# Optimization experiments

Measured on AMD Instinct MI355X. Metric: run time of the kernel, lower is better.

Reference implementation:

```python
import jax, jax.numpy as jnp
import numpy as np

B, S, DIM = 4, 2048, 512
HEADS, DHEAD = 8, 64
INNER = HEADS * DHEAD


def setup_inputs() -> dict:
    key = jax.random.key(0)
    k1, k2, k3, k4 = jax.random.split(key, 4)
    x = jax.random.normal(k1, (B, S, DIM), dtype=jnp.float32)
    W_qkv = jax.random.normal(k2, (DIM, 3 * INNER), dtype=jnp.float32) * (DIM ** -0.5)
    W_out = jax.random.normal(k3, (INNER, DIM), dtype=jnp.float32) * (INNER ** -0.5)
    b_out = jnp.zeros((DIM,), dtype=jnp.float32)
    # learnable log-temperature, initialized to log(dim_head**-0.5)
    log_temp = jnp.asarray(np.log(DHEAD ** -0.5), dtype=jnp.float32)
    return {"x": x, "W_qkv": W_qkv, "log_temp": log_temp, "W_out": W_out, "b_out": b_out}


def reference(x, W_qkv, log_temp, W_out, b_out):
    b, s, _ = x.shape
    qkv = x @ W_qkv  # [b, s, 3*inner]
    q, k, v = jnp.split(qkv, 3, axis=-1)
    # [b, s, inner] -> [b, h, s, d]
    reshape = lambda t: t.reshape(b, s, HEADS, DHEAD).transpose(0, 2, 1, 3)
    q, k, v = reshape(q), reshape(k), reshape(v)
    dots = jnp.einsum("bhid,bhjd->bhij", q, k) * jnp.exp(log_temp)
    mask_value = -jnp.finfo(dots.dtype).max
    eye = jnp.eye(s, dtype=bool)
    dots = jnp.where(eye, mask_value, dots)
    attn = jax.nn.softmax(dots, axis=-1)
    out = jnp.einsum("bhij,bhjd->bhid", attn, v)
    out = out.transpose(0, 2, 1, 3).reshape(b, s, INNER)
    return out @ W_out + b_out
```

## Files before the change

### kernel.cpp

```cpp
#include <hip/hip_runtime.h>
#include <hip/hip_bf16.h>

#define BB 4
#define SS 2048
#define DIMM 512
#define HH 8
#define DD 64
#define NQKV 1536

typedef float  floatx4 __attribute__((ext_vector_type(4)));
typedef short  bf16x8  __attribute__((ext_vector_type(8)));
typedef short  bf16x4  __attribute__((ext_vector_type(4)));

#define MFMA16(A, B, C) __builtin_amdgcn_mfma_f32_16x16x32_bf16(A, B, C, 0, 0, 0)

__device__ __forceinline__ floatx4 MFMA16K16(bf16x4 a, bf16x4 b, floatx4 c) {
#if __has_builtin(__builtin_amdgcn_mfma_f32_16x16x16bf16_1k)
    return __builtin_amdgcn_mfma_f32_16x16x16bf16_1k(a, b, c, 0, 0, 0);
#else
    floatx4 d;
    asm volatile("v_mfma_f32_16x16x16_bf16 %0, %1, %2, %3"
                 : "=v"(d) : "v"(a), "v"(b), "v"(c));
    return d;
#endif
}

__device__ __forceinline__ unsigned short f2bf(float f) {
    unsigned int u = __float_as_uint(f);
    u += 0x7FFFu + ((u >> 16) & 1u);
    return (unsigned short)(u >> 16);
}

__device__ __forceinline__ unsigned int f2bf_pk(float lo, float hi) {
    float2 f; f.x = lo; f.y = hi;
    __hip_bfloat162 h = __float22bfloat162_rn(f);
    return *reinterpret_cast<unsigned int*>(&h);
}

__device__ __forceinline__ float fast_exp2(float x) {
#if __has_builtin(__builtin_amdgcn_exp2f)
    return __builtin_amdgcn_exp2f(x);
#else
    return __exp2f(x);
#endif
}

__device__ __forceinline__ void gl_lds16(const void* g, void* l) {
    __builtin_amdgcn_global_load_lds(
        (__attribute__((address_space(1))) void*)g,
        (__attribute__((address_space(3))) void*)l,
        16, 0, 0);
}

__global__ __launch_bounds__(256) void k_prep(
    const float* __restrict__ x, const float* __restrict__ W_qkv,
    const float* __restrict__ W_out,
    unsigned short* __restrict__ xb, unsigned short* __restrict__ Wq_t,
    unsigned short* __restrict__ Wo_t) {
    __shared__ float t[32][33];
    int bid = blockIdx.x, tid = threadIdx.x;
    if (bid < 4096) {
        int i = (bid * 256 + tid) * 4;
        float4 v = *(const float4*)(x + i);
        ushort4 o;
        o.x = f2bf(v.x); o.y = f2bf(v.y); o.z = f2bf(v.z); o.w = f2bf(v.w);
        *(ushort4*)(xb + i) = o;
        return;
    }
    const float* in; unsigned short* out; int R = 512, C, bx, by;
    if (bid < 4864) { in = W_qkv; out = Wq_t; C = 1536; int blk = bid - 4096; bx = blk % 48; by = blk / 48; }
    else            { in = W_out; out = Wo_t; C = 512;  int blk = bid - 4864; bx = blk % 16; by = blk / 16; }
    int tx = tid & 31, ty = tid >> 5;
    int c0 = bx * 32, r0 = by * 32;
    for (int i = 0; i < 4; i++) {
        int r = r0 + ty + i * 8;
        t[ty + i * 8][tx] = in[(size_t)r * C + c0 + tx];
    }
    __syncthreads();
    for (int i = 0; i < 4; i++) {
        int cc = c0 + ty + i * 8;
        out[(size_t)cc * R + r0 + tx] = f2bf(t[tx][ty + i * 8]);
    }
}

__global__ __launch_bounds__(256) void k_gemm_qkv(
    const unsigned short* __restrict__ A,
    const unsigned short* __restrict__ Bt,
    const float* __restrict__ log_temp,
    unsigned short* __restrict__ Qb,
    unsigned short* __restrict__ Kb,
    unsigned short* __restrict__ Vt) {
    __shared__ unsigned short smem[2][128 * 64];
    unsigned short* As = smem[0];
    unsigned short* Bs = smem[1];
    const int K = 512;
    int m0 = blockIdx.x * 128, n0 = blockIdx.y * 128;
    int tid = threadIdx.x;
    int w = tid >> 6, lane = tid & 63;
    int c = lane & 15, q4 = lane >> 4;
    int wm = w >> 1, wn = w & 1;
    float qscale = __expf(log_temp[0]) * 1.44269504f;

    floatx4 acc[4][4] = {};

    for (int k0 = 0; k0 < K; k0 += 64) {
        __syncthreads();
        for (int i = 0; i < 4; i++) {
            int cidx = w * 256 + i * 64 + lane;
            int row = cidx >> 3, cc = cidx & 7;
            int gcc = cc ^ (row & 7);
            gl_lds16(A + (size_t)(m0 + row) * K + k0 + gcc * 8,
                     As + (size_t)(w * 256 + i * 64) * 8);
            gl_lds16(Bt + (size_t)(n0 + row) * K + k0 + gcc * 8,
                     Bs + (size_t)(w * 256 + i * 64) * 8);
        }
        __syncthreads();
        bf16x8 aF[2][4], bF[2][4];
        for (int kh = 0; kh < 2; kh++)
            for (int mt = 0; mt < 4; mt++) {
                int row = wm * 64 + mt * 16 + c;
                aF[kh][mt] = *(const bf16x8*)&As[row * 64 + (((kh * 4 + q4) ^ (row & 7)) * 8)];
            }
        for (int kh = 0; kh < 2; kh++)
            for (int nt = 0; nt < 4; nt++) {
                int row = wn * 64 + nt * 16 + c;
                bF[kh][nt] = *(const bf16x8*)&Bs[row * 64 + (((kh * 4 + q4) ^ (row & 7)) * 8)];
            }
        for (int kh = 0; kh < 2; kh++)
            for (int mt = 0; mt < 4; mt++)
                for (int nt = 0; nt < 4; nt++)
                    acc[mt][nt] = MFMA16(aF[kh][mt], bF[kh][nt], acc[mt][nt]);
    }

    if (n0 < 1024) {
        for (int nt = 0; nt < 4; nt++) {
            int n = n0 + wn * 64 + nt * 16 + c;
            int t = n >> 9, inner = n & 511;
            int h = inner >> 6, d = inner & 63;
            for (int mt = 0; mt < 4; mt++) {
                for (int r = 0; r < 4; r++) {
                    int m = m0 + wm * 64 + mt * 16 + q4 * 4 + r;
                    int b = m >> 11, s = m & 2047;
                    int bh = b * 8 + h;
                    float v = acc[mt][nt][r];
                    if (t == 0)  Qb[((size_t)bh * SS + s) * 64 + d] = f2bf(v * qscale);
                    else         Kb[((size_t)bh * SS + s) * 64 + d] = f2bf(v);
                }
            }
        }
    } else {
        unsigned short* T = &smem[0][0];
        int b = m0 >> 11, s_base = m0 & 2047;
        for (int half = 0; half < 2; half++) {
            __syncthreads();
            if (wn == half) {
                for (int nt = 0; nt < 4; nt++)
                    for (int mt = 0; mt < 4; mt++)
                        for (int r = 0; r < 4; r++)
                            T[(nt * 16 + c) * 136 + wm * 64 + mt * 16 + q4 * 4 + r] =
                                f2bf(acc[mt][nt][r]);
            }
            __syncthreads();
            for (int rr = 0; rr < 4; rr++) {
                int nl = w * 16 + rr * 4 + q4;
                int ml = c * 8;
                bf16x8 v = *(const bf16x8*)&T[nl * 136 + ml];
                int n = n0 + half * 64 + nl;
                int h = (n >> 6) - 16, d = n & 63;
                int bh = b * 8 + h;
                *(bf16x8*)(Vt + ((size_t)bh * 64 + d) * SS + s_base + ml) = v;
            }
        }
    }
}

__global__ __launch_bounds__(512, 4) void k_attn(
    const unsigned short* __restrict__ Qb,
    const unsigned short* __restrict__ Kb,
    const unsigned short* __restrict__ Vt,
    unsigned short* __restrict__ AO) {
    __shared__ unsigned short Ks[2][64 * 64];
    __shared__ unsigned short Vs[2][64 * 64];
    int q0 = blockIdx.x * 128;
    int h = blockIdx.y, b = blockIdx.z;
    int bh = b * 8 + h;
    int tid = threadIdx.x, w = tid >> 6, lane = tid & 63;
    int c = lane & 15, q4 = lane >> 4;

    const unsigned short* Kbase = Kb + (size_t)bh * SS * 64;
    const unsigned short* Vbase = Vt + (size_t)bh * 64 * SS;

    bf16x8 qf[2];
    {
        const unsigned short* qp = Qb + ((size_t)bh * SS + q0 + w * 16 + c) * 64;
        qf[0] = *(const bf16x8*)(qp + q4 * 8);
        qf[1] = *(const bf16x8*)(qp + 32 + q4 * 8);
    }

    int grow = tid >> 3, gcc = (tid & 7) ^ (grow & 7);
    const unsigned short* ksrc = Kbase + (size_t)grow * 64 + gcc * 8;
    const unsigned short* vsrc = Vbase + (size_t)grow * SS + gcc * 8;
    unsigned short* kdst = (unsigned short*)Ks[0] + w * 512;
    unsigned short* vdst = (unsigned short*)Vs[0] + w * 512;

    gl_lds16(ksrc, kdst);
    gl_lds16(vsrc, vdst);

    int mask_j0 = (q0 + w * 16) & ~63;
    int mglob = q0 + w * 16 + c;
    floatx4 oacc[4] = {};
    float psum = 0.f;

    for (int j0 = 0; j0 < SS; j0 += 64) {
        int buf = (j0 >> 6) & 1;
        __syncthreads();
        if (j0 + 64 < SS) {
            gl_lds16(ksrc + (size_t)(j0 + 64) * 64, kdst + (buf ^ 1) * 4096);
            gl_lds16(vsrc + (j0 + 64), vdst + (buf ^ 1) * 4096);
        }
        bool diag = (j0 == mask_j0);

        for (int jt = 0; jt < 4; jt++) {
            int row = jt * 16 + c;
            bf16x8 kf0 = *(const bf16x8*)&Ks[buf][row * 64 + ((q4 ^ (row & 7)) * 8)];
            bf16x8 kf1 = *(const bf16x8*)&Ks[buf][row * 64 + (((4 + q4) ^ (row & 7)) * 8)];
            floatx4 sa = {};
            sa = MFMA16(kf0, qf[0], sa);
            sa = MFMA16(kf1, qf[1], sa);

            if (diag) {
                for (int r = 0; r < 4; r++) {
                    int jg = j0 + jt * 16 + q4 * 4 + r;
                    if (jg == mglob) sa[r] = -1e30f;
                }
            }

            float e0 = fast_exp2(sa[0]), e1 = fast_exp2(sa[1]);
            float e2 = fast_exp2(sa[2]), e3 = fast_exp2(sa[3]);
            psum += (e0 + e1) + (e2 + e3);
            union { bf16x4 v; unsigned int u[2]; } P;
            P.u[0] = f2bf_pk(e0, e1); P.u[1] = f2bf_pk(e2, e3);

            int chunk = jt * 2 + (q4 >> 1);
            int sub = (q4 & 1) * 4;
            for (int dt = 0; dt < 4; dt++) {
                int vrow = dt * 16 + c;
                bf16x4 vf = *(const bf16x4*)&Vs[buf][vrow * 64 + ((chunk ^ (vrow & 7)) * 8) + sub];
                oacc[dt] = MFMA16K16(P.v, vf, oacc[dt]);
            }
        }
    }

    float l = psum;
    l += __shfl_xor(l, 16);
    l += __shfl_xor(l, 32);
    for (int r = 0; r < 4; r++) {
        float lr = __shfl(l, q4 * 4 + r, 64);
        float inv = 1.0f / lr;
        int s = q0 + w * 16 + q4 * 4 + r;
        for (int dt = 0; dt < 4; dt++)
            AO[((size_t)b * SS + s) * 512 + h * 64 + dt * 16 + c] =
                f2bf(oacc[dt][r] * inv);
    }
}

__global__ __launch_bounds__(256) void k_gemm_out(
    const unsigned short* __restrict__ A,
    const unsigned short* __restrict__ Bt,
    const float* __restrict__ bias,
    float* __restrict__ out) {
    __shared__ unsigned short As[64 * 64];
    __shared__ unsigned short Bs[128 * 64];
    const int K = 512;
    int m0 = blockIdx.x * 64, n0 = blockIdx.y * 128;
    int tid = threadIdx.x;
    int w = tid >> 6, lane = tid & 63;
    int c = lane & 15, q4 = lane >> 4;

    floatx4 acc[8] = {};

    for (int k0 = 0; k0 < K; k0 += 64) {
        __syncthreads();
        for (int i = 0; i < 2; i++) {
            int cidx = i * 256 + tid;
            int row = cidx >> 3, cc = cidx & 7;
            int gcc = cc ^ (row & 7);
            gl_lds16(A + (size_t)(m0 + row) * K + k0 + gcc * 8,
                     As + (size_t)(i * 256 + w * 64) * 8);
        }
        for (int i = 0; i < 4; i++) {
            int cidx = i * 256 + tid;
            int row = cidx >> 3, cc = cidx & 7;
            int gcc = cc ^ (row & 7);
            gl_lds16(Bt + (size_t)(n0 + row) * K + k0 + gcc * 8,
                     Bs + (size_t)(i * 256 + w * 64) * 8);
        }
        __syncthreads();
        bf16x8 aF[2], bF[2][8];
        for (int kh = 0; kh < 2; kh++) {
            int row = w * 16 + c;
            aF[kh] = *(const bf16x8*)&As[row * 64 + (((kh * 4 + q4) ^ (row & 7)) * 8)];
        }
        for (int kh = 0; kh < 2; kh++)
            for (int nt = 0; nt < 8; nt++) {
                int row = nt * 16 + c;
                bF[kh][nt] = *(const bf16x8*)&Bs[row * 64 + (((kh * 4 + q4) ^ (row & 7)) * 8)];
            }
        for (int kh = 0; kh < 2; kh++)
            for (int nt = 0; nt < 8; nt++)
                acc[nt] = MFMA16(aF[kh], bF[kh][nt], acc[nt]);
    }

    for (int nt = 0; nt < 8; nt++) {
        int n = n0 + nt * 16 + c;
        float bv = bias[n];
        for (int r = 0; r < 4; r++) {
            int m = m0 + w * 16 + q4 * 4 + r;
            out[(size_t)m * 512 + n] = acc[nt][r] + bv;
        }
    }
}

extern "C" void kernel_launch(void* const* d_in, const int* in_sizes, int n_in,
                              void* d_out, int out_size, void* d_ws, size_t ws_size,
                              hipStream_t stream) {
    const float* x        = (const float*)d_in[0];
    const float* W_qkv    = (const float*)d_in[1];
    const float* log_temp = (const float*)d_in[2];
    const float* W_out    = (const float*)d_in[3];
    const float* b_out    = (const float*)d_in[4];
    float* out = (float*)d_out;

    char* ws = (char*)d_ws;
    unsigned short* xb   = (unsigned short*)(ws + 0);
    unsigned short* Wq_t = (unsigned short*)(ws + 8388608);
    unsigned short* Wo_t = (unsigned short*)(ws + 9961472);
    unsigned short* Qb   = (unsigned short*)(ws + 10485760);
    unsigned short* Kb   = (unsigned short*)(ws + 18874368);
    unsigned short* Vt   = (unsigned short*)(ws + 27262976);
    unsigned short* AO   = (unsigned short*)(ws + 35651584);

    k_prep<<<5120, 256, 0, stream>>>(x, W_qkv, W_out, xb, Wq_t, Wo_t);
    k_gemm_qkv<<<dim3(64, 12), 256, 0, stream>>>(xb, Wq_t, log_temp, Qb, Kb, Vt);
    k_attn<<<dim3(16, 8, 4), 512, 0, stream>>>(Qb, Kb, Vt, AO);
    k_gemm_out<<<dim3(128, 4), 256, 0, stream>>>(AO, Wo_t, b_out, out);
}
```

Baseline: 164.6 us.

## Process two query tiles per wave in attention to reuse K/V LDS loads

Each wave in the attention kernel now handles 32 query rows (two 16-row MFMA tiles) instead of 16, so every K and V fragment read from LDS feeds twice as many MFMAs. The block covers 256 queries, the grid is halved to 256 blocks, and launch bounds drop to 2 blocks per CU to leave room for the larger accumulator set. This cuts LDS traffic and global K/V staging per query. In exchange it uses more registers and launches fewer blocks, which on a 256-CU part may leave the machine less full.

```diff
diff --git a/kernel.cpp b/kernel.cpp
--- a/kernel.cpp
+++ b/kernel.cpp
@@ -174,14 +174,14 @@
     }
 }
 
-__global__ __launch_bounds__(512, 4) void k_attn(
+__global__ __launch_bounds__(512, 2) void k_attn(
     const unsigned short* __restrict__ Qb,
     const unsigned short* __restrict__ Kb,
     const unsigned short* __restrict__ Vt,
     unsigned short* __restrict__ AO) {
     __shared__ unsigned short Ks[2][64 * 64];
     __shared__ unsigned short Vs[2][64 * 64];
-    int q0 = blockIdx.x * 128;
+    int q0 = blockIdx.x * 256;
     int h = blockIdx.y, b = blockIdx.z;
     int bh = b * 8 + h;
     int tid = threadIdx.x, w = tid >> 6, lane = tid & 63;
@@ -190,11 +190,11 @@
     const unsigned short* Kbase = Kb + (size_t)bh * SS * 64;
     const unsigned short* Vbase = Vt + (size_t)bh * 64 * SS;
 
-    bf16x8 qf[2];
-    {
-        const unsigned short* qp = Qb + ((size_t)bh * SS + q0 + w * 16 + c) * 64;
-        qf[0] = *(const bf16x8*)(qp + q4 * 8);
-        qf[1] = *(const bf16x8*)(qp + 32 + q4 * 8);
+    bf16x8 qf[2][2];
+    for (int mi = 0; mi < 2; mi++) {
+        const unsigned short* qp = Qb + ((size_t)bh * SS + q0 + w * 32 + mi * 16 + c) * 64;
+        qf[mi][0] = *(const bf16x8*)(qp + q4 * 8);
+        qf[mi][1] = *(const bf16x8*)(qp + 32 + q4 * 8);
     }
 
     int grow = tid >> 3, gcc = (tid & 7) ^ (grow & 7);
@@ -206,10 +206,16 @@
     gl_lds16(ksrc, kdst);
     gl_lds16(vsrc, vdst);
 
-    int mask_j0 = (q0 + w * 16) & ~63;
-    int mglob = q0 + w * 16 + c;
-    floatx4 oacc[4] = {};
-    float psum = 0.f;
+    int koff0 = (q4 ^ (c & 7)) * 8;
+    int koff1 = ((4 + q4) ^ (c & 7)) * 8;
+    int vsub = (q4 & 1) * 4;
+    int vchunk0 = (q4 >> 1);
+
+    int mask_j0 = (q0 + w * 32) & ~63;
+    int mglob0 = q0 + w * 32 + c;
+    int mglob1 = mglob0 + 16;
+    floatx4 oacc[2][4] = {};
+    float psum0 = 0.f, psum1 = 0.f;
 
     for (int j0 = 0; j0 < SS; j0 += 64) {
         int buf = (j0 >> 6) & 1;
@@ -219,48 +225,63 @@
             gl_lds16(vsrc + (j0 + 64), vdst + (buf ^ 1) * 4096);
         }
         bool diag = (j0 == mask_j0);
-
+        const unsigned short* KsB = Ks[buf];
+        const unsigned short* VsB = Vs[buf];
+
+#pragma unroll
         for (int jt = 0; jt < 4; jt++) {
-            int row = jt * 16 + c;
-            bf16x8 kf0 = *(const bf16x8*)&Ks[buf][row * 64 + ((q4 ^ (row & 7)) * 8)];
-            bf16x8 kf1 = *(const bf16x8*)&Ks[buf][row * 64 + (((4 + q4) ^ (row & 7)) * 8)];
-            floatx4 sa = {};
-            sa = MFMA16(kf0, qf[0], sa);
-            sa = MFMA16(kf1, qf[1], sa);
+            int rowoff = (jt * 16 + c) * 64;
+            bf16x8 kf0 = *(const bf16x8*)&KsB[rowoff + koff0];
+            bf16x8 kf1 = *(const bf16x8*)&KsB[rowoff + koff1];
+            floatx4 sa0 = {}, sa1 = {};
+            sa0 = MFMA16(kf0, qf[0][0], sa0);
+            sa0 = MFMA16(kf1, qf[0][1], sa0);
+            sa1 = MFMA16(kf0, qf[1][0], sa1);
+            sa1 = MFMA16(kf1, qf[1][1], sa1);
 
             if (diag) {
+#pragma unroll
                 for (int r = 0; r < 4; r++) {
                     int jg = j0 + jt * 16 + q4 * 4 + r;
-                    if (jg == mglob) sa[r] = -1e30f;
+                    if (jg == mglob0) sa0[r] = -1e30f;
+                    if (jg == mglob1) sa1[r] = -1e30f;
                 }
             }
 
-            float e0 = fast_exp2(sa[0]), e1 = fast_exp2(sa[1]);
-            float e2 = fast_exp2(sa[2]), e3 = fast_exp2(sa[3]);
-            psum += (e0 + e1) + (e2 + e3);
-            union { bf16x4 v; unsigned int u[2]; } P;
-            P.u[0] = f2bf_pk(e0, e1); P.u[1] = f2bf_pk(e2, e3);
-
-            int chunk = jt * 2 + (q4 >> 1);
-            int sub = (q4 & 1) * 4;
+            float e0 = fast_exp2(sa0[0]), e1 = fast_exp2(sa0[1]);
+            float e2 = fast_exp2(sa0[2]), e3 = fast_exp2(sa0[3]);
+            psum0 += (e0 + e1) + (e2 + e3);
+            union { bf16x4 v; unsigned int u[2]; } P0;
+            P0.u[0] = f2bf_pk(e0, e1); P0.u[1] = f2bf_pk(e2, e3);
+            float f0 = fast_exp2(sa1[0]), f1 = fast_exp2(sa1[1]);
+            float f2v = fast_exp2(sa1[2]), f3 = fast_exp2(sa1[3]);
+            psum1 += (f0 + f1) + (f2v + f3);
+            union { bf16x4 v; unsigned int u[2]; } P1;
+            P1.u[0] = f2bf_pk(f0, f1); P1.u[1] = f2bf_pk(f2v, f3);
+
+            int chunk = jt * 2 + vchunk0;
+#pragma unroll
             for (int dt = 0; dt < 4; dt++) {
                 int vrow = dt * 16 + c;
-                bf16x4 vf = *(const bf16x4*)&Vs[buf][vrow * 64 + ((chunk ^ (vrow & 7)) * 8) + sub];
-                oacc[dt] = MFMA16K16(P.v, vf, oacc[dt]);
-            }
-        }
-    }
-
-    float l = psum;
-    l += __shfl_xor(l, 16);
-    l += __shfl_xor(l, 32);
-    for (int r = 0; r < 4; r++) {
-        float lr = __shfl(l, q4 * 4 + r, 64);
-        float inv = 1.0f / lr;
-        int s = q0 + w * 16 + q4 * 4 + r;
-        for (int dt = 0; dt < 4; dt++)
-            AO[((size_t)b * SS + s) * 512 + h * 64 + dt * 16 + c] =
-                f2bf(oacc[dt][r] * inv);
+                bf16x4 vf = *(const bf16x4*)&VsB[vrow * 64 + ((chunk ^ (c & 7)) * 8) + vsub];
+                oacc[0][dt] = MFMA16K16(P0.v, vf, oacc[0][dt]);
+                oacc[1][dt] = MFMA16K16(P1.v, vf, oacc[1][dt]);
+            }
+        }
+    }
+
+    for (int mi = 0; mi < 2; mi++) {
+        float l = (mi == 0) ? psum0 : psum1;
+        l += __shfl_xor(l, 16);
+        l += __shfl_xor(l, 32);
+        for (int r = 0; r < 4; r++) {
+            float lr = __shfl(l, q4 * 4 + r, 64);
+            float inv = 1.0f / lr;
+            int s = q0 + w * 32 + mi * 16 + q4 * 4 + r;
+            for (int dt = 0; dt < 4; dt++)
+                AO[((size_t)b * SS + s) * 512 + h * 64 + dt * 16 + c] =
+                    f2bf(oacc[mi][dt][r] * inv);
+        }
     }
 }
 
@@ -342,6 +363,6 @@
 
     k_prep<<<5120, 256, 0, stream>>>(x, W_qkv, W_out, xb, Wq_t, Wo_t);
     k_gemm_qkv<<<dim3(64, 12), 256, 0, stream>>>(xb, Wq_t, log_temp, Qb, Kb, Vt);
-    k_attn<<<dim3(16, 8, 4), 512, 0, stream>>>(Qb, Kb, Vt, AO);
+    k_attn<<<dim3(8, 8, 4), 512, 0, stream>>>(Qb, Kb, Vt, AO);
     k_gemm_out<<<dim3(128, 4), 256, 0, stream>>>(AO, Wo_t, b_out, out);
 }
```

Result: slower. 168.2 us (+2.2%).
